# Kernel tuning notes

Hardware: AMD Instinct MI355X
Metric: run time of the kernel (lower is better)

The kernel has to match this reference:

```python
import jax, jax.numpy as jnp
import numpy as np

B, S, L, D = 128, 256, 200, 768
POS_VOCAB, POS_DIM = 60, 50
REDUC, HID, TAGS, POL = 400, 150, 5, 4


def setup_inputs() -> dict:
    key = jax.random.key(0)
    ks = jax.random.split(key, 12)
    bert_vectors = jax.random.normal(ks[0], (B, S, D), dtype=jnp.float32)
    # ragged subword spans: word j covers subwords [start_j, end_j] (inclusive), length 1..3,
    # skipping the [CLS] token at index 0. Clipped to S-1 (long sentences just truncate).
    rng = np.random.default_rng(0)
    lens = rng.integers(1, 4, size=(B, L))
    cum = np.cumsum(lens, axis=1)
    starts = 1 + cum - lens
    ends = cum
    starts = np.minimum(starts, S - 1)
    ends = np.minimum(ends, S - 1)
    ends = np.maximum(ends, starts)
    positions = jnp.asarray(np.stack([starts, ends], axis=-1), dtype=jnp.int32)
    postag = jax.random.randint(ks[1], (B, L), 1, POS_VOCAB).astype(jnp.int32)

    def lin(k, o, i):
        return jax.random.normal(k, (o, i), jnp.float32) / np.float32(np.sqrt(i))

    return dict(
        bert_vectors=bert_vectors,
        positions=positions,
        postag=postag,
        embed_table=jax.random.normal(ks[2], (POS_VOCAB, POS_DIM), jnp.float32) * 0.02,
        W_reduc=lin(ks[3], REDUC, D + POS_DIM), b_reduc=jnp.zeros((REDUC,), jnp.float32),
        W_ap=lin(ks[4], HID, REDUC), b_ap=jnp.zeros((HID,), jnp.float32),
        W_op=lin(ks[5], HID, REDUC), b_op=jnp.zeros((HID,), jnp.float32),
        W_ap2=lin(ks[6], HID, REDUC), b_ap2=jnp.zeros((HID,), jnp.float32),
        W_op2=lin(ks[7], HID, REDUC), b_op2=jnp.zeros((HID,), jnp.float32),
        W_aptag=lin(ks[8], TAGS, HID), b_aptag=jnp.zeros((TAGS,), jnp.float32),
        W_optag=lin(ks[9], TAGS, HID), b_optag=jnp.zeros((TAGS,), jnp.float32),
        W_bi=lin(ks[10], POL * HID, HID + 1),
    )


def _pool_subwords(vectors, positions):
    # variable-length mean pooling of subword vectors into word vectors
    # vectors: [B,S,D], positions: [B,L,2] -> [B,L,D]
    idx = jnp.arange(S)[None, None, :]                      # [1,1,S]
    p0 = positions[..., 0][..., None]                       # [B,L,1]
    p1 = positions[..., 1][..., None]
    m = ((idx >= p0) & (idx <= p1)).astype(vectors.dtype)   # [B,L,S]
    cnt = jnp.maximum(m.sum(-1, keepdims=True), 1.0)
    return jnp.einsum('bls,bsd->bld', m, vectors) / cnt


def reference(bert_vectors, positions, postag, embed_table,
              W_reduc, b_reduc, W_ap, b_ap, W_op, b_op,
              W_ap2, b_ap2, W_op2, b_op2,
              W_aptag, b_aptag, W_optag, b_optag, W_bi):
    word_vecs = _pool_subwords(bert_vectors, positions)                 # [B,L,D]
    pos_emb = embed_table[postag]                                       # [B,L,50]
    h = jnp.concatenate([pos_emb, word_vecs], axis=-1)                  # [B,L,D+50]
    reduc = jnp.einsum('blf,of->blo', h, W_reduc) + b_reduc             # [B,L,400]
    ap_rep = jax.nn.relu(jnp.einsum('blf,of->blo', reduc, W_ap) + b_ap)
    op_rep = jax.nn.relu(jnp.einsum('blf,of->blo', reduc, W_op) + b_op)
    ap_node = jax.nn.relu(jnp.einsum('blf,of->blo', reduc, W_ap2) + b_ap2)
    op_node = jax.nn.relu(jnp.einsum('blf,of->blo', reduc, W_op2) + b_op2)
    ap_out = jnp.einsum('blf,of->blo', ap_rep, W_aptag) + b_aptag       # [B,L,5]
    op_out = jnp.einsum('blf,of->blo', op_rep, W_optag) + b_optag       # [B,L,5]
    # Biaffine(150,150,POL,bias=(True,False))
    ones = jnp.ones((B, L, 1), ap_node.dtype)
    in1 = jnp.concatenate([ap_node, ones], axis=-1)                     # [B,L,151]
    affine = jnp.einsum('bli,oi->blo', in1, W_bi).reshape(B, L * POL, HID)
    tri = jnp.einsum('bkh,bmh->bkm', affine, op_node)                   # [B,L*POL,L]
    triplet_out = tri.transpose(0, 2, 1).reshape(B, L, L, POL)          # [B,L2,L1,POL]
    return (ap_out, op_out, triplet_out)
```

## Files before the change

### kernel.cpp

```cpp
#include <hip/hip_runtime.h>
#include <hip/hip_bf16.h>

#define Bsz 128
#define Ssz 256
#define Lsz 200
#define Dsz 768
#define POS_DIM 50
#define TAGS 5
#define NROW 25600
#define FIN 818
#define KH 832
#define KR 416
#define KD 160

typedef __attribute__((ext_vector_type(8))) short short8;
typedef __attribute__((ext_vector_type(4))) float floatx4;

__device__ __forceinline__ short f2bf(float v) {
    __hip_bfloat16 h = __float2bfloat16(v);
    short s; __builtin_memcpy(&s, &h, 2); return s;
}
__device__ __forceinline__ float bf2f(short s) {
    __hip_bfloat16 h; __builtin_memcpy(&h, &s, 2);
    return __bfloat162float(h);
}

__device__ __forceinline__ void gload16(const short* g, short* l) {
    __builtin_amdgcn_global_load_lds(
        (const __attribute__((address_space(1))) void*)g,
        (__attribute__((address_space(3))) void*)l, 16, 0, 0);
}

__global__ void prep_kernel(const float* __restrict__ W_reduc,
                            const float* __restrict__ W_ap, const float* __restrict__ W_op,
                            const float* __restrict__ W_ap2, const float* __restrict__ W_op2,
                            const float* __restrict__ W_bi,
                            const float* __restrict__ b_reduc,
                            const float* __restrict__ b_ap, const float* __restrict__ b_op,
                            const float* __restrict__ b_ap2, const float* __restrict__ b_op2,
                            short* __restrict__ Wr_bf, short* __restrict__ Wh_bf,
                            short* __restrict__ Wbi_bf,
                            float* __restrict__ br_pad, float* __restrict__ bh_pad,
                            float* __restrict__ bbi_pad)
{
    int i = blockIdx.x * blockDim.x + threadIdx.x;
    if (i < 512 * KH) {
        int r = i / KH, c = i % KH;
        Wr_bf[i] = (r < 400 && c < FIN) ? f2bf(W_reduc[r * FIN + c]) : (short)0;
    }
    if (i < 640 * KR) {
        int r = i / KR, c = i % KR;
        float v = 0.0f;
        if (r < 600 && c < 400) {
            const float* src = (r < 150) ? W_ap : (r < 300) ? W_op : (r < 450) ? W_ap2 : W_op2;
            v = src[(r % 150) * 400 + c];
        }
        Wh_bf[i] = f2bf(v);
    }
    if (i < 640 * KD) {
        int r = i / KD, c = i % KD;
        Wbi_bf[i] = (r < 600 && c < 150) ? f2bf(W_bi[r * 151 + c]) : (short)0;
    }
    if (i < KR) br_pad[i] = (i < 400) ? b_reduc[i] : 0.0f;
    if (i < 640) {
        float v = 0.0f;
        if (i < 600) {
            const float* bs = (i < 150) ? b_ap : (i < 300) ? b_op : (i < 450) ? b_ap2 : b_op2;
            v = bs[i % 150];
        }
        bh_pad[i] = v;
        bbi_pad[i] = (i < 600) ? W_bi[i * 151 + 150] : 0.0f;
    }
}

__global__ void pool_kernel(const float* __restrict__ bert,
                            const int* __restrict__ positions,
                            const int* __restrict__ postag,
                            const float* __restrict__ embed,
                            short* __restrict__ h_bf)
{
    int row = blockIdx.x;
    int b = row / Lsz;
    int st = positions[row * 2 + 0];
    int en = positions[row * 2 + 1];
    int tag = postag[row];
    int span = en - st + 1;
    float inv = 1.0f / (float)span;
    const float* base = bert + ((long)b * Ssz + st) * Dsz;
    short* hr = h_bf + (long)row * KH;
    for (int f = threadIdx.x; f < KH; f += blockDim.x) {
        float v = 0.0f;
        if (f < POS_DIM) {
            v = embed[tag * POS_DIM + f];
        } else if (f < FIN) {
            int d = f - POS_DIM;
            float s = 0.0f;
            for (int i = 0; i < span; ++i) s += base[i * Dsz + d];
            v = s * inv;
        }
        hr[f] = f2bf(v);
    }
}

__global__ __launch_bounds__(256) void gemm_mfma(
    const short* __restrict__ A, long long sAb, int lda,
    const short* __restrict__ Bt, long long sBb, int ldb,
    const float* __restrict__ bias,
    short* __restrict__ outB, float* __restrict__ outF, long long sCb, int ldc,
    int M, int Nv, int K, int mode)
{
    __shared__ __align__(16) short AB[8192];

    int bz = blockIdx.z;
    A += (long long)bz * sAb;
    Bt += (long long)bz * sBb;

    int row0 = blockIdx.y * 128;
    int col0 = blockIdx.x * 128;
    int tid = threadIdx.x;
    int lane = tid & 63;
    int wv = tid >> 6;
    int wr = wv >> 1, wc = wv & 1;
    int lm = lane & 15, lk = lane >> 4;

    int s0 = tid, s1 = tid + 256;
    int am0 = s0 & 127, ak0 = s0 >> 7;
    int am1 = s1 & 127, ak1 = s1 >> 7;
    const short* gA0 = A + (long)(row0 + am0) * lda + ak0 * 8;
    const short* gA1 = A + (long)(row0 + am1) * lda + ak1 * 8;
    const short* gB0 = Bt + (long)(col0 + am0) * ldb + ak0 * 8;
    const short* gB1 = Bt + (long)(col0 + am1) * ldb + ak1 * 8;
    short* lA0 = &AB[s0 * 8];
    short* lA1 = &AB[s1 * 8];
    short* lB0 = &AB[4096 + s0 * 8];
    short* lB1 = &AB[4096 + s1 * 8];

    const short* fA = &AB[(lk * 128 + wr * 64 + lm) * 8];
    const short* fB = &AB[4096 + (lk * 128 + wc * 64 + lm) * 8];

    floatx4 acc[4][4];
#pragma unroll
    for (int i = 0; i < 4; ++i)
#pragma unroll
        for (int j = 0; j < 4; ++j)
            acc[i][j] = (floatx4){0.f, 0.f, 0.f, 0.f};

    for (int k0 = 0; k0 < K; k0 += 32) {
        gload16(gA0 + k0, lA0);
        gload16(gA1 + k0, lA1);
        gload16(gB0 + k0, lB0);
        gload16(gB1 + k0, lB1);
        __syncthreads();
        short8 a[4], b[4];
#pragma unroll
        for (int mt = 0; mt < 4; ++mt) a[mt] = *(const short8*)(fA + mt * 128);
#pragma unroll
        for (int nt = 0; nt < 4; ++nt) b[nt] = *(const short8*)(fB + nt * 128);
#pragma unroll
        for (int mt = 0; mt < 4; ++mt)
#pragma unroll
            for (int nt = 0; nt < 4; ++nt)
                acc[mt][nt] = __builtin_amdgcn_mfma_f32_16x16x32_bf16(
                    a[mt], b[nt], acc[mt][nt], 0, 0, 0);
        __syncthreads();
    }

#pragma unroll
    for (int mt = 0; mt < 4; ++mt) {
#pragma unroll
        for (int nt = 0; nt < 4; ++nt) {
#pragma unroll
            for (int r = 0; r < 4; ++r) {
                int gm = row0 + wr * 64 + mt * 16 + (lane >> 4) * 4 + r;
                int gn = col0 + wc * 64 + nt * 16 + (lane & 15);
                float v = acc[mt][nt][r];
                if (mode == 0) {
                    if (gn < Nv)
                        outB[(long)gm * ldc + gn] = f2bf(v + bias[gn]);
                } else if (mode == 1) {
                    if (gn < 600) {
                        v = fmaxf(v + bias[gn], 0.0f);
                        outB[((long)(gn / 150) * NROW + gm) * KD + gn % 150] = f2bf(v);
                    } else if (gn < 640) {
                        int q = gn - 600;
                        outB[((long)(q / 10) * NROW + gm) * KD + 150 + q % 10] = 0;
                    }
                } else if (mode == 2) {
                    int bb = gm / 200, l = gm % 200;
                    if (gn < 600) {
                        v += bias[gn];
                        outB[((long)bb * 800 + l * 4 + gn / 150) * KD + gn % 150] = f2bf(v);
                    } else if (gn < 640) {
                        int q = gn - 600;
                        outB[((long)bb * 800 + l * 4 + q / 10) * KD + 150 + q % 10] = 0;
                    }
                } else {
                    if (gm < M && gn < Nv)
                        outF[(long long)bz * sCb + (long)gm * ldc + gn] = v;
                }
            }
        }
    }
}

__global__ __launch_bounds__(256) void tags_kernel(
    const short* __restrict__ hid4,
    const float* __restrict__ W_aptag, const float* __restrict__ b_aptag,
    const float* __restrict__ W_optag, const float* __restrict__ b_optag,
    float* __restrict__ out_ap, float* __restrict__ out_op)
{
    int wave = threadIdx.x / 64;
    int lane = threadIdx.x % 64;
    int row = blockIdx.x * 4 + wave;
    if (row >= NROW) return;

#pragma unroll
    for (int which = 0; which < 2; ++which) {
        const short* rep = hid4 + ((long)which * NROW + row) * KD;
        const float* W = which ? W_optag : W_aptag;
        const float* bb = which ? b_optag : b_aptag;
        float* out = which ? out_op : out_ap;
        float v0 = bf2f(rep[lane]);
        float v1 = bf2f(rep[64 + lane]);
        float v2 = (lane < 22) ? bf2f(rep[128 + lane]) : 0.0f;
#pragma unroll
        for (int t = 0; t < TAGS; ++t) {
            const float* w = W + t * 150;
            float p = v0 * w[lane] + v1 * w[64 + lane] +
                      ((lane < 22) ? v2 * w[128 + lane] : 0.0f);
#pragma unroll
            for (int off = 32; off > 0; off >>= 1) p += __shfl_down(p, off);
            if (lane == 0) out[row * TAGS + t] = p + bb[t];
        }
    }
}

extern "C" void kernel_launch(void* const* d_in, const int* in_sizes, int n_in,
                              void* d_out, int out_size, void* d_ws, size_t ws_size,
                              hipStream_t stream)
{
    const float* bert      = (const float*)d_in[0];
    const int*   positions = (const int*)d_in[1];
    const int*   postag    = (const int*)d_in[2];
    const float* embed     = (const float*)d_in[3];
    const float* W_reduc   = (const float*)d_in[4];
    const float* b_reduc   = (const float*)d_in[5];
    const float* W_ap      = (const float*)d_in[6];
    const float* b_ap      = (const float*)d_in[7];
    const float* W_op      = (const float*)d_in[8];
    const float* b_op      = (const float*)d_in[9];
    const float* W_ap2     = (const float*)d_in[10];
    const float* b_ap2     = (const float*)d_in[11];
    const float* W_op2     = (const float*)d_in[12];
    const float* b_op2     = (const float*)d_in[13];
    const float* W_aptag   = (const float*)d_in[14];
    const float* b_aptag   = (const float*)d_in[15];
    const float* W_optag   = (const float*)d_in[16];
    const float* b_optag   = (const float*)d_in[17];
    const float* W_bi      = (const float*)d_in[18];

    float* out = (float*)d_out;
    float* out_ap  = out;
    float* out_op  = out + NROW * TAGS;
    float* out_tri = out + 2 * NROW * TAGS;

    short* ws = (short*)d_ws;
    short* h_bf     = ws;
    short* affine   = h_bf;
    short* reduc_bf = h_bf + (long)NROW * KH;
    short* hid4     = reduc_bf + (long)NROW * KR;
    short* Wr_bf    = hid4 + (long)4 * NROW * KD;
    short* Wh_bf    = Wr_bf + 512 * KH;
    short* Wbi_bf   = Wh_bf + 640 * KR;
    float* br_pad   = (float*)(Wbi_bf + 640 * KD);
    float* bh_pad   = br_pad + KR;
    float* bbi_pad  = bh_pad + 640;

    prep_kernel<<<(512 * KH + 255) / 256, 256, 0, stream>>>(
        W_reduc, W_ap, W_op, W_ap2, W_op2, W_bi,
        b_reduc, b_ap, b_op, b_ap2, b_op2,
        Wr_bf, Wh_bf, Wbi_bf, br_pad, bh_pad, bbi_pad);

    pool_kernel<<<NROW, 256, 0, stream>>>(bert, positions, postag, embed, h_bf);

    {
        dim3 g(4, NROW / 128, 1);
        gemm_mfma<<<g, 256, 0, stream>>>(h_bf, 0, KH, Wr_bf, 0, KH, br_pad,
                                         reduc_bf, nullptr, 0, KR,
                                         NROW, KR, KH, 0);
    }
    {
        dim3 g(5, NROW / 128, 1);
        gemm_mfma<<<g, 256, 0, stream>>>(reduc_bf, 0, KR, Wh_bf, 0, KR, bh_pad,
                                         hid4, nullptr, 0, 0,
                                         NROW, 600, KR, 1);
    }
    tags_kernel<<<NROW / 4, 256, 0, stream>>>(hid4, W_aptag, b_aptag,
                                              W_optag, b_optag, out_ap, out_op);
    {
        dim3 g(5, NROW / 128, 1);
        gemm_mfma<<<g, 256, 0, stream>>>(hid4 + (long)2 * NROW * KD, 0, KD,
                                         Wbi_bf, 0, KD, bbi_pad,
                                         affine, nullptr, 0, 0,
                                         NROW, 600, KD, 2);
    }
    {
        dim3 g(7, 2, Bsz);
        gemm_mfma<<<g, 256, 0, stream>>>(hid4 + (long)3 * NROW * KD, (long long)200 * KD, KD,
                                         affine, (long long)800 * KD, KD, nullptr,
                                         nullptr, out_tri, (long long)200 * 800, 800,
                                         200, 800, KD, 3);
    }
}
```

Measured before the change: 513.5 us.

## Shrink GEMM tile to 64x128, vectorize pooling and reorder reduc feature layout

The GEMM block tile drops from 128x128 to 64x128, so each of the four waves now owns a 64x32 slice. This doubles the grid size for better CU occupancy and load balance, and shrinks per-wave accumulator registers, at the cost of less operand reuse per block. The pooling kernel now has each thread handle four contiguous bert features with float4 loads and a single vector store. To keep these reads aligned, the POS embedding moves to the end of the h row, and the W_reduc column permutation in prep is changed to match.

```diff
diff --git a/kernel.cpp b/kernel.cpp
--- a/kernel.cpp
+++ b/kernel.cpp
@@ -14,6 +14,7 @@
 #define KD 160
 
 typedef __attribute__((ext_vector_type(8))) short short8;
+typedef __attribute__((ext_vector_type(4))) short short4v;
 typedef __attribute__((ext_vector_type(4))) float floatx4;
 
 __device__ __forceinline__ short f2bf(float v) {
@@ -45,8 +46,13 @@
 {
     int i = blockIdx.x * blockDim.x + threadIdx.x;
     if (i < 512 * KH) {
-        int r = i / KH, c = i % KH;
-        Wr_bf[i] = (r < 400 && c < FIN) ? f2bf(W_reduc[r * FIN + c]) : (short)0;
+        int r = i / KH, k = i % KH;
+        float v = 0.0f;
+        if (r < 400) {
+            if (k < 768)       v = W_reduc[r * FIN + POS_DIM + k];
+            else if (k < 818)  v = W_reduc[r * FIN + (k - 768)];
+        }
+        Wr_bf[i] = f2bf(v);
     }
     if (i < 640 * KR) {
         int r = i / KR, c = i % KR;
@@ -73,11 +79,12 @@
     }
 }
 
-__global__ void pool_kernel(const float* __restrict__ bert,
-                            const int* __restrict__ positions,
-                            const int* __restrict__ postag,
-                            const float* __restrict__ embed,
-                            short* __restrict__ h_bf)
+__global__ __launch_bounds__(256) void pool_kernel(
+    const float* __restrict__ bert,
+    const int* __restrict__ positions,
+    const int* __restrict__ postag,
+    const float* __restrict__ embed,
+    short* __restrict__ h_bf)
 {
     int row = blockIdx.x;
     int b = row / Lsz;
@@ -88,18 +95,29 @@
     float inv = 1.0f / (float)span;
     const float* base = bert + ((long)b * Ssz + st) * Dsz;
     short* hr = h_bf + (long)row * KH;
-    for (int f = threadIdx.x; f < KH; f += blockDim.x) {
-        float v = 0.0f;
-        if (f < POS_DIM) {
-            v = embed[tag * POS_DIM + f];
-        } else if (f < FIN) {
-            int d = f - POS_DIM;
-            float s = 0.0f;
-            for (int i = 0; i < span; ++i) s += base[i * Dsz + d];
-            v = s * inv;
-        }
-        hr[f] = f2bf(v);
-    }
+
+    int t = threadIdx.x;
+    int c0 = t * 4;
+    if (c0 >= KH) return;
+    short4v o;
+    if (c0 < 768) {
+        float4 s = {0.f, 0.f, 0.f, 0.f};
+        for (int i = 0; i < span; ++i) {
+            float4 v = *(const float4*)(base + i * Dsz + c0);
+            s.x += v.x; s.y += v.y; s.z += v.z; s.w += v.w;
+        }
+        o.x = f2bf(s.x * inv); o.y = f2bf(s.y * inv);
+        o.z = f2bf(s.z * inv); o.w = f2bf(s.w * inv);
+    } else {
+        const float* e = embed + tag * POS_DIM;
+#pragma unroll
+        for (int j = 0; j < 4; ++j) {
+            int c = c0 + j - 768;
+            float v = (c < POS_DIM) ? e[c] : 0.0f;
+            ((short*)&o)[j] = f2bf(v);
+        }
+    }
+    *(short4v*)(hr + c0) = o;
 }
 
 __global__ __launch_bounds__(256) void gemm_mfma(
@@ -109,57 +127,51 @@
     short* __restrict__ outB, float* __restrict__ outF, long long sCb, int ldc,
     int M, int Nv, int K, int mode)
 {
-    __shared__ __align__(16) short AB[8192];
+    __shared__ __align__(16) short AB[6144];
 
     int bz = blockIdx.z;
     A += (long long)bz * sAb;
     Bt += (long long)bz * sBb;
 
-    int row0 = blockIdx.y * 128;
+    int row0 = blockIdx.y * 64;
     int col0 = blockIdx.x * 128;
     int tid = threadIdx.x;
     int lane = tid & 63;
     int wv = tid >> 6;
-    int wr = wv >> 1, wc = wv & 1;
     int lm = lane & 15, lk = lane >> 4;
 
-    int s0 = tid, s1 = tid + 256;
-    int am0 = s0 & 127, ak0 = s0 >> 7;
-    int am1 = s1 & 127, ak1 = s1 >> 7;
-    const short* gA0 = A + (long)(row0 + am0) * lda + ak0 * 8;
-    const short* gA1 = A + (long)(row0 + am1) * lda + ak1 * 8;
-    const short* gB0 = Bt + (long)(col0 + am0) * ldb + ak0 * 8;
-    const short* gB1 = Bt + (long)(col0 + am1) * ldb + ak1 * 8;
-    short* lA0 = &AB[s0 * 8];
-    short* lA1 = &AB[s1 * 8];
-    short* lB0 = &AB[4096 + s0 * 8];
-    short* lB1 = &AB[4096 + s1 * 8];
-
-    const short* fA = &AB[(lk * 128 + wr * 64 + lm) * 8];
-    const short* fB = &AB[4096 + (lk * 128 + wc * 64 + lm) * 8];
-
-    floatx4 acc[4][4];
+    const short* gA0 = A + (long)(row0 + (tid & 63)) * lda + (tid >> 6) * 8;
+    int bc0 = tid, bc1 = tid + 256;
+    const short* gB0 = Bt + (long)(col0 + (bc0 & 127)) * ldb + (bc0 >> 7) * 8;
+    const short* gB1 = Bt + (long)(col0 + (bc1 & 127)) * ldb + (bc1 >> 7) * 8;
+    short* lA0 = &AB[tid * 8];
+    short* lB0 = &AB[2048 + bc0 * 8];
+    short* lB1 = &AB[2048 + bc1 * 8];
+
+    const short* fA = &AB[(lk * 64 + lm) * 8];
+    const short* fB = &AB[2048 + (lk * 128 + wv * 32 + lm) * 8];
+
+    floatx4 acc[4][2];
 #pragma unroll
     for (int i = 0; i < 4; ++i)
 #pragma unroll
-        for (int j = 0; j < 4; ++j)
+        for (int j = 0; j < 2; ++j)
             acc[i][j] = (floatx4){0.f, 0.f, 0.f, 0.f};
 
     for (int k0 = 0; k0 < K; k0 += 32) {
         gload16(gA0 + k0, lA0);
-        gload16(gA1 + k0, lA1);
         gload16(gB0 + k0, lB0);
         gload16(gB1 + k0, lB1);
         __syncthreads();
-        short8 a[4], b[4];
+        short8 a[4], b[2];
 #pragma unroll
         for (int mt = 0; mt < 4; ++mt) a[mt] = *(const short8*)(fA + mt * 128);
 #pragma unroll
-        for (int nt = 0; nt < 4; ++nt) b[nt] = *(const short8*)(fB + nt * 128);
+        for (int nt = 0; nt < 2; ++nt) b[nt] = *(const short8*)(fB + nt * 128);
 #pragma unroll
         for (int mt = 0; mt < 4; ++mt)
 #pragma unroll
-            for (int nt = 0; nt < 4; ++nt)
+            for (int nt = 0; nt < 2; ++nt)
                 acc[mt][nt] = __builtin_amdgcn_mfma_f32_16x16x32_bf16(
                     a[mt], b[nt], acc[mt][nt], 0, 0, 0);
         __syncthreads();
@@ -168,11 +180,11 @@
 #pragma unroll
     for (int mt = 0; mt < 4; ++mt) {
 #pragma unroll
-        for (int nt = 0; nt < 4; ++nt) {
+        for (int nt = 0; nt < 2; ++nt) {
 #pragma unroll
             for (int r = 0; r < 4; ++r) {
-                int gm = row0 + wr * 64 + mt * 16 + (lane >> 4) * 4 + r;
-                int gn = col0 + wc * 64 + nt * 16 + (lane & 15);
+                int gm = row0 + mt * 16 + lk * 4 + r;
+                int gn = col0 + wv * 32 + nt * 16 + lm;
                 float v = acc[mt][nt][r];
                 if (mode == 0) {
                     if (gn < Nv)
@@ -284,13 +296,13 @@
     pool_kernel<<<NROW, 256, 0, stream>>>(bert, positions, postag, embed, h_bf);
 
     {
-        dim3 g(4, NROW / 128, 1);
+        dim3 g(4, NROW / 64, 1);
         gemm_mfma<<<g, 256, 0, stream>>>(h_bf, 0, KH, Wr_bf, 0, KH, br_pad,
                                          reduc_bf, nullptr, 0, KR,
                                          NROW, KR, KH, 0);
     }
     {
-        dim3 g(5, NROW / 128, 1);
+        dim3 g(5, NROW / 64, 1);
         gemm_mfma<<<g, 256, 0, stream>>>(reduc_bf, 0, KR, Wh_bf, 0, KR, bh_pad,
                                          hid4, nullptr, 0, 0,
                                          NROW, 600, KR, 1);
@@ -298,14 +310,14 @@
     tags_kernel<<<NROW / 4, 256, 0, stream>>>(hid4, W_aptag, b_aptag,
                                               W_optag, b_optag, out_ap, out_op);
     {
-        dim3 g(5, NROW / 128, 1);
+        dim3 g(5, NROW / 64, 1);
         gemm_mfma<<<g, 256, 0, stream>>>(hid4 + (long)2 * NROW * KD, 0, KD,
                                          Wbi_bf, 0, KD, bbi_pad,
                                          affine, nullptr, 0, 0,
                                          NROW, 600, KD, 2);
     }
     {
-        dim3 g(7, 2, Bsz);
+        dim3 g(7, 4, Bsz);
         gemm_mfma<<<g, 256, 0, stream>>>(hid4 + (long)3 * NROW * KD, (long long)200 * KD, KD,
                                          affine, (long long)800 * KD, KD, nullptr,
                                          nullptr, out_tri, (long long)200 * 800, 800,
```

After: 469.8 us. -8.5%, faster.
